# Kernel tuning notes

Measured on AMD Instinct MI355X. Metric: run time of the kernel, lower is better.

Reference implementation:

```python
import jax, jax.numpy as jnp
import numpy as np

NUM_HEADS = 16
NUM_KV_HEADS = 8
HEAD_DIM = 128
GATE_LOW_RANK = 16
GATE_NORMALIZER = 16.0
NORM_EPS = 1e-5
CHUNK = 64


def gla_chunk(q, k, v, g, chunk=CHUNK):
    """Chunkwise-parallel gated linear attention.
    q,k,v,g: [B,H,L,D]. Recurrence: S_t = diag(exp(g_t)) S_{t-1} + k_t^T v_t; o_t = q_t S_t.
    """
    B, H, L, D = q.shape
    n = L // chunk

    def rs(x):  # -> [n, B, H, C, D]
        return x.reshape(B, H, n, chunk, D).transpose(2, 0, 1, 3, 4)

    qc, kc, vc, gc = rs(q), rs(k), rs(v), rs(g)
    causal = jnp.tril(jnp.ones((chunk, chunk), dtype=bool))

    def step(S, inp):
        qt, kt, vt, gt = inp                      # [B,H,C,D]
        b = jnp.cumsum(gt, axis=-2)               # inclusive cumulative log-gates
        q_ = qt * jnp.exp(b)
        k_ = kt * jnp.exp(-b)
        # intra-chunk causal attention (diag included)
        A = jnp.einsum('bhid,bhjd->bhij', q_, k_)
        A = jnp.where(causal, A, 0.0)
        o = jnp.einsum('bhij,bhje->bhie', A, vt)
        # inter-chunk contribution from carried state
        o = o + jnp.einsum('bhid,bhde->bhie', q_, S)
        # state update to end of chunk
        k_end = kt * jnp.exp(b[..., -1:, :] - b)
        S_new = S * jnp.exp(b[..., -1, :])[..., None] + jnp.einsum('bhcd,bhce->bhde', k_end, vt)
        return S_new, o

    S0 = jnp.zeros((B, H, D, D), q.dtype)
    _, o = jax.lax.scan(step, S0, (qc, kc, vc, gc))
    return o.transpose(1, 2, 0, 3, 4).reshape(B, H, L, D)


def setup_inputs() -> dict:
    key = jax.random.key(0)
    ks = jax.random.split(key, 10)
    B, L, HID = 2, 2048, 2048
    KV = NUM_KV_HEADS * HEAD_DIM  # 1024
    w = 0.02
    return {
        'hidden_states': jax.random.normal(ks[0], (B, L, HID), jnp.float32),
        'Wq': jax.random.normal(ks[1], (HID, HID), jnp.float32) * w,
        'bq': jnp.zeros((HID,), jnp.float32),
        'Wk': jax.random.normal(ks[2], (HID, KV), jnp.float32) * w,
        'bk': jnp.zeros((KV,), jnp.float32),
        'Wv': jax.random.normal(ks[3], (HID, KV), jnp.float32) * w,
        'bv': jnp.zeros((KV,), jnp.float32),
        'Wg1': jax.random.normal(ks[4], (HID, GATE_LOW_RANK), jnp.float32) * w,
        'Wg2': jax.random.normal(ks[5], (GATE_LOW_RANK, KV), jnp.float32) * w,
        'bg2': jnp.zeros((KV,), jnp.float32),
        'g_norm_w': jnp.ones((HEAD_DIM,), jnp.float32),
        'Wo': jax.random.normal(ks[6], (HID, HID), jnp.float32) * w,
    }


def reference(hidden_states, Wq, bq, Wk, bk, Wv, bv, Wg1, Wg2, bg2, g_norm_w, Wo):
    B, L, HID = hidden_states.shape
    H, HKV, D = NUM_HEADS, NUM_KV_HEADS, HEAD_DIM
    n_rep = H // HKV

    q = jax.nn.relu(hidden_states @ Wq + bq)          # feature_map = relu
    k = jax.nn.relu(hidden_states @ Wk + bk)
    v = hidden_states @ Wv + bv
    gk = jax.nn.log_sigmoid((hidden_states @ Wg1) @ Wg2 + bg2) / GATE_NORMALIZER

    q = q.reshape(B, L, H, D).transpose(0, 2, 1, 3)    # [B,H,L,D]
    def to_heads(x):
        return x.reshape(B, L, HKV, D).transpose(0, 2, 1, 3)
    k, v, gk = to_heads(k), to_heads(v), to_heads(gk)  # [B,HKV,L,D]
    # GQA: repeat kv heads
    k = jnp.repeat(k, n_rep, axis=1)
    v = jnp.repeat(v, n_rep, axis=1)
    gk = jnp.repeat(gk, n_rep, axis=1)

    q = q * (D ** -0.5)                                # scale as in chunk_gla
    o = gla_chunk(q, k, v, gk)                         # [B,H,L,D]

    # per-head RMSNorm over head_dim
    o = o * jax.lax.rsqrt(jnp.mean(o * o, axis=-1, keepdims=True) + NORM_EPS) * g_norm_w
    o = o.transpose(0, 2, 1, 3).reshape(B, L, H * D)
    return o @ Wo
```

## Files before the change

kernel.cpp:

```cpp
#include <hip/hip_runtime.h>

typedef unsigned short u16;
typedef u16 u16x8 __attribute__((ext_vector_type(8)));
typedef u16 u16x4 __attribute__((ext_vector_type(4)));
typedef __bf16 bf16x8 __attribute__((ext_vector_type(8)));
typedef float f32x4 __attribute__((ext_vector_type(4)));

#define DEVI static __device__ __forceinline__

DEVI float b2f(u16 u){ union { unsigned u; float f; } c; c.u = ((unsigned)u) << 16; return c.f; }
DEVI u16 f2b(float f){ union { float f; unsigned u; } c; c.f = f;
  unsigned r = c.u + 0x7fffu + ((c.u >> 16) & 1u); return (u16)(r >> 16); }
DEVI void gload16(const void* g, void* l){
  __builtin_amdgcn_global_load_lds((const __attribute__((address_space(1))) void*)g,
                                   (__attribute__((address_space(3))) void*)l, 16, 0, 0);
}
DEVI f32x4 MFMA(bf16x8 a, bf16x8 b, f32x4 c){
  return __builtin_amdgcn_mfma_f32_16x16x32_bf16(a, b, c, 0, 0, 0);
}
#define WAITV(n) asm volatile("s_waitcnt vmcnt(" #n ")" ::: "memory")
#define WAITL0() asm volatile("s_waitcnt lgkmcnt(0)" ::: "memory")

constexpr size_t OFF_HB  = 0;
constexpr size_t OFF_WCT = OFF_HB  + (size_t)4096*2048*2;
constexpr size_t OFF_WOT = OFF_WCT + (size_t)4224*2048*2;
constexpr size_t OFF_QKV = OFF_WOT + (size_t)2048*2048*2;
constexpr size_t OFF_G1  = OFF_QKV + (size_t)4096*4096*2;
constexpr size_t OFF_G   = OFF_G1  + (size_t)4096*16*4;
constexpr size_t OFF_EB  = OFF_G   + (size_t)4096*1024*4;
constexpr size_t OFF_KD  = OFF_EB  + (size_t)4096*1024*2;
constexpr size_t OFF_T   = OFF_KD  + (size_t)4096*1024*2;
constexpr size_t OFF_DV  = OFF_T   + (size_t)2*8*32*128*128*2;
constexpr size_t OFF_SP  = OFF_DV  + (size_t)2*8*32*128*4;
constexpr size_t OFF_ON  = OFF_SP  + (size_t)2*8*32*128*128*2;

__global__ __launch_bounds__(256) void k_conv_h(const float* __restrict__ h, u16* __restrict__ hb){
  int idx = blockIdx.x*256 + threadIdx.x, stride = gridDim.x*256;
  for (int i = idx; i < 4096*2048/4; i += stride){
    float4 v = ((const float4*)h)[i];
    u16x4 o; o[0]=f2b(v.x); o[1]=f2b(v.y); o[2]=f2b(v.z); o[3]=f2b(v.w);
    ((u16x4*)hb)[i] = o;
  }
}

__global__ __launch_bounds__(256) void k_transpose(const float* __restrict__ src, u16* __restrict__ dst,
                                                   int K, int N, int rowOff, int pitch){
  __shared__ float tile[64][65];
  int kb = blockIdx.y*64, nb = blockIdx.x*64;
  int t = threadIdx.x, x = t & 63, y0 = t >> 6;
#pragma unroll
  for (int i = 0; i < 16; i++){
    int y = y0 + i*4, k = kb + y, n = nb + x;
    tile[y][x] = (n < N) ? src[(size_t)k*N + n] : 0.f;
  }
  __syncthreads();
#pragma unroll
  for (int i = 0; i < 16; i++){
    int y = y0 + i*4, n = nb + y, k = kb + x;
    if (n < N) dst[(size_t)(rowOff + n)*pitch + k] = f2b(tile[x][y]);
  }
}

__global__ __launch_bounds__(256) void k_wtilde(const float* __restrict__ Wg1, const float* __restrict__ Wg2,
                                                u16* __restrict__ wt){
  __shared__ float w2s[16*8];
  int c0 = blockIdx.x*8, t = threadIdx.x;
  if (t < 128){ int j = t>>3, cc = t&7; w2s[j*8+cc] = Wg2[j*1024 + c0 + cc]; }
  __syncthreads();
  int r0 = t*8;
#pragma unroll
  for (int half = 0; half < 2; half++){
    float rowv[4][16];
#pragma unroll
    for (int u = 0; u < 4; u++)
#pragma unroll
      for (int j4 = 0; j4 < 4; j4++)
        *(float4*)&rowv[u][j4*4] = *(const float4*)&Wg1[(size_t)(r0 + half*4 + u)*16 + j4*4];
#pragma unroll
    for (int cc = 0; cc < 8; cc++){
      u16x4 o;
#pragma unroll
      for (int u = 0; u < 4; u++){
        float s = 0.f;
#pragma unroll
        for (int j = 0; j < 16; j++) s += rowv[u][j]*w2s[j*8+cc];
        o[u] = f2b(s);
      }
      *(u16x4*)&wt[(size_t)(c0+cc)*2048 + r0 + half*4] = o;
    }
  }
}

template<int BM, int MODE>
__global__ __launch_bounds__(512, 2) void gemm256(const u16* __restrict__ A, const u16* __restrict__ Bt,
                                                  u16* __restrict__ Cq, float* __restrict__ Cf,
                                                  const float* __restrict__ bq, const float* __restrict__ bk,
                                                  const float* __restrict__ bv){
  constexpr int NT = 64;
  constexpr int MI = BM/32;
  constexpr int ALOADS = BM/128;
  constexpr int NTN = (MODE==0) ? 16 : 8;
  __shared__ u16 sA[4*BM*32];
  __shared__ u16 sB[4*256*32];
  int id = blockIdx.x;
  int swz = (id & 7)*32 + (id >> 3);
  int mt = swz / NTN, nt = swz % NTN;
  int t = threadIdx.x, w = t >> 6, l = t & 63;
  int wr = w >> 2, wc = w & 3;
  int mRow0 = mt*BM, nCol0 = nt*256;
  const u16* srcA[ALOADS]; const u16* srcB[2];
#pragma unroll
  for (int i = 0; i < ALOADS; i++){
    int S = t + i*512, r = S>>2, g = (S&3) ^ ((r>>1)&3);
    srcA[i] = A + (size_t)(mRow0 + r)*2048 + g*8;
  }
#pragma unroll
  for (int i = 0; i < 2; i++){
    int S = t + i*512, r = S>>2, g = (S&3) ^ ((r>>1)&3);
    srcB[i] = Bt + (size_t)(nCol0 + r)*2048 + g*8;
  }
  auto ISSUE = [&](int T){
    int buf = T & 3;
    u16* dA = sA + buf*(BM*32);
    u16* dB = sB + buf*(256*32);
#pragma unroll
    for (int i = 0; i < ALOADS; i++) gload16(srcA[i] + T*32, dA + (i*512 + w*64)*8);
#pragma unroll
    for (int i = 0; i < 2; i++)      gload16(srcB[i] + T*32, dB + (i*512 + w*64)*8);
  };
  f32x4 acc[MI][4] = {};
  ISSUE(0); ISSUE(1); ISSUE(2);
  for (int T = 0; T < NT; ++T){
    if (T + 3 < NT) ISSUE(T + 3);
    if constexpr (BM == 256){
      if (T < NT-3)       WAITV(12);
      else if (T == NT-3) WAITV(8);
      else if (T == NT-2) WAITV(4);
      else                WAITV(0);
    } else {
      if (T < NT-3)       WAITV(9);
      else if (T == NT-3) WAITV(6);
      else if (T == NT-2) WAITV(3);
      else                WAITV(0);
    }
    __builtin_amdgcn_s_barrier();
    const u16* bufA = sA + (T&3)*(BM*32);
    const u16* bufB = sB + (T&3)*(256*32);
    bf16x8 bfr[4], afr[MI];
#pragma unroll
    for (int ni = 0; ni < 4; ni++){
      int r = wc*64 + ni*16 + (l&15);
      int p = (l>>4) ^ ((r>>1)&3);
      bfr[ni] = *(const bf16x8*)&bufB[(r*4 + p)*8];
    }
#pragma unroll
    for (int mi = 0; mi < MI; mi++){
      int r = wr*(BM/2) + mi*16 + (l&15);
      int p = (l>>4) ^ ((r>>1)&3);
      afr[mi] = *(const bf16x8*)&bufA[(r*4 + p)*8];
    }
    __builtin_amdgcn_s_setprio(1);
#pragma unroll
    for (int mi = 0; mi < MI; mi++)
#pragma unroll
      for (int ni = 0; ni < 4; ni++)
        acc[mi][ni] = MFMA(afr[mi], bfr[ni], acc[mi][ni]);
    __builtin_amdgcn_s_setprio(0);
    WAITL0();
    __builtin_amdgcn_s_barrier();
  }
  int iLoc = (l>>4)*4, jc = l & 15;
  if (MODE == 0){
#pragma unroll
    for (int ni = 0; ni < 4; ni++){
      int n0 = nCol0 + wc*64 + ni*16;
      int n = n0 + jc;
      int kind; float bias;
      if (n0 < 2048){ kind = 0; bias = bq[n]; }
      else if (n0 < 3072){ kind = 1; bias = bk[n - 2048]; }
      else { kind = 2; bias = bv[n - 3072]; }
#pragma unroll
      for (int mi = 0; mi < MI; mi++){
        int m = mRow0 + wr*(BM/2) + mi*16 + iLoc;
#pragma unroll
        for (int rr = 0; rr < 4; rr++){
          float x = acc[mi][ni][rr] + bias;
          int row = m + rr;
          if (kind == 0)      Cq[(size_t)row*4096 + n] = f2b(fmaxf(x, 0.f) * 0.08838834764831845f);
          else if (kind == 1) Cq[(size_t)row*4096 + n] = f2b(fmaxf(x, 0.f));
          else                Cq[(size_t)row*4096 + n] = f2b(x);
        }
      }
    }
  } else {
#pragma unroll
    for (int ni = 0; ni < 4; ni++){
      int n = nCol0 + wc*64 + ni*16 + jc;
#pragma unroll
      for (int mi = 0; mi < MI; mi++){
        int m = mRow0 + wr*(BM/2) + mi*16 + iLoc;
#pragma unroll
        for (int rr = 0; rr < 4; rr++) Cf[(size_t)(m+rr)*2048 + n] = acc[mi][ni][rr];
      }
    }
  }
}

__global__ __launch_bounds__(256, 2) void gemmG(const u16* __restrict__ A, const u16* __restrict__ Bt,
                                                float* __restrict__ Cg, const float* __restrict__ bg2){
  constexpr int NT = 64;
  __shared__ u16 sA[4*128*32];
  __shared__ u16 sB[4*128*32];
  int id = blockIdx.x;
  int swz = (id & 7)*32 + (id >> 3);
  int mt = swz >> 3, nt = swz & 7;
  int t = threadIdx.x, w = t >> 6, l = t & 63;
  int wr = w >> 1, wc = w & 1;
  int mRow0 = mt*128, nCol0 = nt*128;
  const u16* srcA[2]; const u16* srcB[2];
#pragma unroll
  for (int i = 0; i < 2; i++){
    int S = t + i*256, r = S>>2, g = (S&3) ^ ((r>>1)&3);
    srcA[i] = A + (size_t)(mRow0 + r)*2048 + g*8;
    srcB[i] = Bt + (size_t)(nCol0 + r)*2048 + g*8;
  }
  auto ISSUE = [&](int T){
    int buf = T & 3;
    u16* dA = sA + buf*4096;
    u16* dB = sB + buf*4096;
#pragma unroll
    for (int i = 0; i < 2; i++) gload16(srcA[i] + T*32, dA + (i*256 + w*64)*8);
#pragma unroll
    for (int i = 0; i < 2; i++) gload16(srcB[i] + T*32, dB + (i*256 + w*64)*8);
  };
  f32x4 acc[4][4] = {};
  ISSUE(0); ISSUE(1); ISSUE(2);
  for (int T = 0; T < NT; ++T){
    if (T + 3 < NT) ISSUE(T + 3);
    if (T < NT-3)       WAITV(12);
    else if (T == NT-3) WAITV(8);
    else if (T == NT-2) WAITV(4);
    else                WAITV(0);
    __builtin_amdgcn_s_barrier();
    const u16* bufA = sA + (T&3)*4096;
    const u16* bufB = sB + (T&3)*4096;
    bf16x8 bfr[4], afr[4];
#pragma unroll
    for (int ni = 0; ni < 4; ni++){
      int r = wc*64 + ni*16 + (l&15);
      int p = (l>>4) ^ ((r>>1)&3);
      bfr[ni] = *(const bf16x8*)&bufB[(r*4 + p)*8];
    }
#pragma unroll
    for (int mi = 0; mi < 4; mi++){
      int r = wr*64 + mi*16 + (l&15);
      int p = (l>>4) ^ ((r>>1)&3);
      afr[mi] = *(const bf16x8*)&bufA[(r*4 + p)*8];
    }
    __builtin_amdgcn_s_setprio(1);
#pragma unroll
    for (int mi = 0; mi < 4; mi++)
#pragma unroll
      for (int ni = 0; ni < 4; ni++)
        acc[mi][ni] = MFMA(afr[mi], bfr[ni], acc[mi][ni]);
    __builtin_amdgcn_s_setprio(0);
    WAITL0();
    __builtin_amdgcn_s_barrier();
  }
  int iLoc = (l>>4)*4, jc = l & 15;
#pragma unroll
  for (int ni = 0; ni < 4; ni++){
    int n = nCol0 + wc*64 + ni*16 + jc;
    float bias = bg2[n];
#pragma unroll
    for (int mi = 0; mi < 4; mi++){
      int m = mRow0 + wr*64 + mi*16 + iLoc;
#pragma unroll
      for (int rr = 0; rr < 4; rr++) Cg[(size_t)(m+rr)*1024 + n] = acc[mi][ni][rr] + bias;
    }
  }
}

__global__ __launch_bounds__(256) void k_phaseA(const float* __restrict__ g, const u16* __restrict__ QKV,
                                                u16* __restrict__ eb, u16* __restrict__ kd,
                                                u16* __restrict__ T, float* __restrict__ Dv){
  __shared__ float gb[64*128];
  __shared__ u16 keT[128*72];
  __shared__ u16 vT [128*72];
  int c = blockIdx.x, kvh = blockIdx.y, b = blockIdx.z;
  int t = threadIdx.x;
  int tok0 = b*2048 + c*64;
#pragma unroll
  for (int r = 0; r < 8; r++){
    int idx4 = r*256 + t;
    int i = idx4 >> 5, c4 = idx4 & 31;
    float4 v = *(const float4*)&g[(size_t)(tok0+i)*1024 + kvh*128 + c4*4];
    float4 o;
    o.x = (fminf(v.x,0.f) - log1pf(expf(-fabsf(v.x)))) * 0.0625f;
    o.y = (fminf(v.y,0.f) - log1pf(expf(-fabsf(v.y)))) * 0.0625f;
    o.z = (fminf(v.z,0.f) - log1pf(expf(-fabsf(v.z)))) * 0.0625f;
    o.w = (fminf(v.w,0.f) - log1pf(expf(-fabsf(v.w)))) * 0.0625f;
    ((float4*)gb)[i*32 + c4] = o;
  }
  __syncthreads();
  if (t < 128){
    float run = 0.f;
    for (int i = 0; i < 64; i++){ run += gb[i*128 + t]; gb[i*128 + t] = run; }
    Dv[((size_t)(b*8+kvh)*32 + c)*128 + t] = expf(run);
  }
  __syncthreads();
  int d0 = (t&15)*8;
  float blast[8];
#pragma unroll
  for (int j = 0; j < 8; j++) blast[j] = gb[63*128 + d0 + j];
#pragma unroll
  for (int r = 0; r < 4; r++){
    int i = (t>>4) + r*16;
    u16x8 kv_ = *(const u16x8*)&QKV[(size_t)(tok0+i)*4096 + 2048 + kvh*128 + d0];
    u16x8 vv  = *(const u16x8*)&QKV[(size_t)(tok0+i)*4096 + 3072 + kvh*128 + d0];
    u16x8 ebv, kdv;
#pragma unroll
    for (int j = 0; j < 8; j++){
      float bcur = gb[i*128 + d0 + j];
      float kf = b2f(kv_[j]);
      ebv[j] = f2b(expf(bcur));
      kdv[j] = f2b(kf * expf(-bcur));
      keT[(d0+j)*72 + i] = f2b(kf * expf(blast[j] - bcur));
      vT [(d0+j)*72 + i] = vv[j];
    }
    *(u16x8*)&eb[(size_t)(tok0+i)*1024 + kvh*128 + d0] = ebv;
    *(u16x8*)&kd[(size_t)(tok0+i)*1024 + kvh*128 + d0] = kdv;
  }
  __syncthreads();
  int w = t>>6, l = t&63;
  f32x4 acc[2][8] = {};
#pragma unroll
  for (int ks = 0; ks < 2; ks++){
    bf16x8 af[2];
#pragma unroll
    for (int ti = 0; ti < 2; ti++)
      af[ti] = *(const bf16x8*)&keT[(w*32 + ti*16 + (l&15))*72 + ks*32 + (l>>4)*8];
#pragma unroll
    for (int tj = 0; tj < 8; tj++){
      bf16x8 bf_ = *(const bf16x8*)&vT[(tj*16 + (l&15))*72 + ks*32 + (l>>4)*8];
#pragma unroll
      for (int ti = 0; ti < 2; ti++) acc[ti][tj] = MFMA(af[ti], bf_, acc[ti][tj]);
    }
  }
  size_t tbase = ((size_t)(b*8+kvh)*32 + c)*16384;
#pragma unroll
  for (int ti = 0; ti < 2; ti++)
#pragma unroll
    for (int tj = 0; tj < 8; tj++)
#pragma unroll
      for (int rr = 0; rr < 4; rr++){
        int d = w*32 + ti*16 + (l>>4)*4 + rr, e = tj*16 + (l&15);
        T[tbase + d*128 + e] = f2b(acc[ti][tj][rr]);
      }
}

__global__ __launch_bounds__(256) void k_phaseB(const u16* __restrict__ T, const float* __restrict__ Dv,
                                                u16* __restrict__ SP){
  __shared__ u16 sl[16*128];
  int es = blockIdx.x, kvh = blockIdx.y, b = blockIdx.z;
  int t = threadIdx.x;
  size_t bh = (size_t)(b*8 + kvh);
  float S[8] = {0,0,0,0,0,0,0,0};
  for (int c = 0; c < 32; c++){
#pragma unroll
    for (int r = 0; r < 8; r++){
      int idx = r*256 + t, d = idx>>4, el = idx&15;
      sl[el*128 + d] = f2b(S[r]);
    }
    __syncthreads();
    size_t spb = (bh*32 + c)*16384 + (size_t)es*2048;
    *(u16x8*)&SP[spb + t*8] = *(const u16x8*)&sl[t*8];
    size_t tb  = (bh*32 + c)*16384;
    size_t dvb = (bh*32 + c)*128;
#pragma unroll
    for (int r = 0; r < 8; r++){
      int idx = r*256 + t, d = idx>>4, el = idx&15;
      float tv = b2f(T[tb + d*128 + es*16 + el]);
      S[r] = S[r]*Dv[dvb + d] + tv;
    }
    __syncthreads();
  }
}

__global__ __launch_bounds__(256) void k_phaseC(const u16* __restrict__ QKV, const u16* __restrict__ eb,
                                                const u16* __restrict__ kd, const u16* __restrict__ SP,
                                                const float* __restrict__ gnw, u16* __restrict__ onrm){
  __shared__ u16 kl[64*128];
  __shared__ u16 sl[64*72];
  __shared__ u16 vT[128*72];
  int c = blockIdx.x, h = blockIdx.y, b = blockIdx.z;
  int kvh = h >> 1;
  int t = threadIdx.x, w = t>>6, l = t&63;
  int tok0 = b*2048 + c*64;
#pragma unroll
  for (int is = 0; is < 4; is++){
    int row = (t>>4) + is*16;
    int d0s = 8*((t&15) ^ (row&7));
    gload16(&kd[(size_t)(tok0+row)*1024 + kvh*128 + d0s], &kl[is*2048 + w*512]);
  }
  int d0v = (t&15)*8;
#pragma unroll
  for (int r = 0; r < 4; r++){
    int i = (t>>4) + r*16;
    u16x8 vv = *(const u16x8*)&QKV[(size_t)(tok0+i)*4096 + 3072 + kvh*128 + d0v];
#pragma unroll
    for (int jj = 0; jj < 8; jj++) vT[(d0v+jj)*72 + i] = vv[jj];
  }
  bf16x8 aq[4];
  {
    int i = w*16 + (l&15);
#pragma unroll
    for (int kt = 0; kt < 4; kt++){
      int dq = kt*32 + (l>>4)*8;
      u16x8 qv = *(const u16x8*)&QKV[(size_t)(tok0+i)*4096 + h*128 + dq];
      u16x8 ev = *(const u16x8*)&eb[(size_t)(tok0+i)*1024 + kvh*128 + dq];
      u16x8 o;
#pragma unroll
      for (int jj = 0; jj < 8; jj++) o[jj] = f2b(b2f(qv[jj]) * b2f(ev[jj]));
      aq[kt] = __builtin_bit_cast(bf16x8, o);
    }
  }
  __syncthreads();
  f32x4 accs[4] = {};
#pragma unroll
  for (int kt = 0; kt < 4; kt++){
#pragma unroll
    for (int jt = 0; jt < 4; jt++){
      int j = jt*16 + (l&15);
      int byte_ = j*256 + ((2*(kt*32 + (l>>4)*8)) ^ ((j&7)<<4));
      bf16x8 bk_ = *(const bf16x8*)((const char*)kl + byte_);
      accs[jt] = MFMA(aq[kt], bk_, accs[jt]);
    }
  }
#pragma unroll
  for (int jt = 0; jt < 4; jt++)
#pragma unroll
    for (int rr = 0; rr < 4; rr++){
      int i = w*16 + (l>>4)*4 + rr;
      int j = jt*16 + (l&15);
      sl[i*72 + j] = f2b((i >= j) ? accs[jt][rr] : 0.f);
    }
  f32x4 acco[8] = {};
  size_t spb = ((size_t)(b*8+kvh)*32 + c)*16384;
#pragma unroll
  for (int kt = 0; kt < 4; kt++){
#pragma unroll
    for (int et = 0; et < 8; et++){
      int e = et*16 + (l&15);
      int dd = kt*32 + (l>>4)*8;
      bf16x8 bs = *(const bf16x8*)&SP[spb + (size_t)e*128 + dd];
      acco[et] = MFMA(aq[kt], bs, acco[et]);
    }
  }
#pragma unroll
  for (int kt2 = 0; kt2 < 2; kt2++){
    int i = w*16 + (l&15);
    bf16x8 as = *(const bf16x8*)&sl[i*72 + kt2*32 + (l>>4)*8];
#pragma unroll
    for (int et = 0; et < 8; et++){
      bf16x8 bv_ = *(const bf16x8*)&vT[(et*16 + (l&15))*72 + kt2*32 + (l>>4)*8];
      acco[et] = MFMA(as, bv_, acco[et]);
    }
  }
  float gw[8];
#pragma unroll
  for (int et = 0; et < 8; et++) gw[et] = gnw[et*16 + (l&15)];
#pragma unroll
  for (int rr = 0; rr < 4; rr++){
    int i = w*16 + (l>>4)*4 + rr;
    float ss = 0.f;
#pragma unroll
    for (int et = 0; et < 8; et++){ float x = acco[et][rr]; ss += x*x; }
    ss += __shfl_xor(ss, 1); ss += __shfl_xor(ss, 2);
    ss += __shfl_xor(ss, 4); ss += __shfl_xor(ss, 8);
    float sc = rsqrtf(ss*(1.f/128.f) + 1e-5f);
#pragma unroll
    for (int et = 0; et < 8; et++){
      int e = et*16 + (l&15);
      onrm[(size_t)(tok0+i)*2048 + h*128 + e] = f2b(acco[et][rr]*sc*gw[et]);
    }
  }
}

extern "C" void kernel_launch(void* const* d_in, const int* in_sizes, int n_in,
                              void* d_out, int out_size, void* d_ws, size_t ws_size,
                              hipStream_t stream){
  (void)in_sizes; (void)n_in; (void)out_size; (void)ws_size;
  const float* h   = (const float*)d_in[0];
  const float* Wq  = (const float*)d_in[1];
  const float* bq  = (const float*)d_in[2];
  const float* Wk  = (const float*)d_in[3];
  const float* bk  = (const float*)d_in[4];
  const float* Wv  = (const float*)d_in[5];
  const float* bv  = (const float*)d_in[6];
  const float* Wg1 = (const float*)d_in[7];
  const float* Wg2 = (const float*)d_in[8];
  const float* bg2 = (const float*)d_in[9];
  const float* gnw = (const float*)d_in[10];
  const float* Wo  = (const float*)d_in[11];
  float* out = (float*)d_out;
  char* ws = (char*)d_ws;
  u16*   hb   = (u16*)  (ws + OFF_HB);
  u16*   wct  = (u16*)  (ws + OFF_WCT);
  u16*   wot  = (u16*)  (ws + OFF_WOT);
  u16*   qkv  = (u16*)  (ws + OFF_QKV);
  float* gbuf = (float*)(ws + OFF_G);
  u16*   ebuf = (u16*)  (ws + OFF_EB);
  u16*   kdb  = (u16*)  (ws + OFF_KD);
  u16*   Tb   = (u16*)  (ws + OFF_T);
  u16*   wtilT= (u16*)  (ws + OFF_T);
  float* Dvb  = (float*)(ws + OFF_DV);
  u16*   SPb  = (u16*)  (ws + OFF_SP);
  u16*   onb  = (u16*)  (ws + OFF_ON);

  k_conv_h<<<2048, 256, 0, stream>>>(h, hb);
  k_transpose<<<dim3(32,32), 256, 0, stream>>>(Wq,  wct, 2048, 2048,    0, 2048);
  k_transpose<<<dim3(16,32), 256, 0, stream>>>(Wk,  wct, 2048, 1024, 2048, 2048);
  k_transpose<<<dim3(16,32), 256, 0, stream>>>(Wv,  wct, 2048, 1024, 3072, 2048);
  k_transpose<<<dim3(32,32), 256, 0, stream>>>(Wo,  wot, 2048, 2048,    0, 2048);
  k_wtilde<<<128, 256, 0, stream>>>(Wg1, Wg2, wtilT);
  gemm256<256,0><<<256, 512, 0, stream>>>(hb, wct, qkv, nullptr, bq, bk, bv);
  gemmG<<<256, 256, 0, stream>>>(hb, wtilT, gbuf, bg2);
  k_phaseA<<<dim3(32,8,2), 256, 0, stream>>>(gbuf, qkv, ebuf, kdb, Tb, Dvb);
  k_phaseB<<<dim3(8,8,2), 256, 0, stream>>>(Tb, Dvb, SPb);
  k_phaseC<<<dim3(32,16,2), 256, 0, stream>>>(qkv, ebuf, kdb, SPb, gnw, onb);
  gemm256<128,1><<<256, 512, 0, stream>>>(onb, wot, nullptr, out, nullptr, nullptr, nullptr);
}
```

Measured before the change: 475.8 us.

## Unify GEMMs into 128x128 double-buffered kernel and transpose state layout for phaseB

Replaces the 256-wide 4-stage GEMM kernels and the separate gate GEMM with one 128x128-tile kernel that uses 256 threads, 2-stage double buffering and __syncthreads, and launches more blocks. Phase A now writes the chunk state transposed (e-major), so phase B can drop its shared-memory transpose and barriers and use vectorized 8-wide loads and stores per thread. The GEMM change trades reuse per block and prefetch depth for occupancy, and may expose more memory latency than the 4-stage pipeline did. Phase C must read the state in the new transposed layout.

```diff
diff --git a/kernel.cpp b/kernel.cpp
--- a/kernel.cpp
+++ b/kernel.cpp
@@ -18,8 +18,6 @@
 DEVI f32x4 MFMA(bf16x8 a, bf16x8 b, f32x4 c){
   return __builtin_amdgcn_mfma_f32_16x16x32_bf16(a, b, c, 0, 0, 0);
 }
-#define WAITV(n) asm volatile("s_waitcnt vmcnt(" #n ")" ::: "memory")
-#define WAITL0() asm volatile("s_waitcnt lgkmcnt(0)" ::: "memory")
 
 constexpr size_t OFF_HB  = 0;
 constexpr size_t OFF_WCT = OFF_HB  + (size_t)4096*2048*2;
@@ -91,62 +89,46 @@
   }
 }
 
-template<int BM, int MODE>
-__global__ __launch_bounds__(512, 2) void gemm256(const u16* __restrict__ A, const u16* __restrict__ Bt,
+template<int MODE>
+__global__ __launch_bounds__(256, 4) void gemm128(const u16* __restrict__ A, const u16* __restrict__ Bt,
                                                   u16* __restrict__ Cq, float* __restrict__ Cf,
                                                   const float* __restrict__ bq, const float* __restrict__ bk,
-                                                  const float* __restrict__ bv){
+                                                  const float* __restrict__ bv, const float* __restrict__ bg2){
   constexpr int NT = 64;
-  constexpr int MI = BM/32;
-  constexpr int ALOADS = BM/128;
-  constexpr int NTN = (MODE==0) ? 16 : 8;
-  __shared__ u16 sA[4*BM*32];
-  __shared__ u16 sB[4*256*32];
+  constexpr int NTN = (MODE==0) ? 32 : (MODE==1) ? 16 : 8;
+  constexpr int CPX = (MODE==0) ? 128 : (MODE==1) ? 64 : 32;
+  __shared__ u16 sA[2*128*32];
+  __shared__ u16 sB[2*128*32];
   int id = blockIdx.x;
-  int swz = (id & 7)*32 + (id >> 3);
+  int swz = (id & 7)*CPX + (id >> 3);
   int mt = swz / NTN, nt = swz % NTN;
   int t = threadIdx.x, w = t >> 6, l = t & 63;
-  int wr = w >> 2, wc = w & 3;
-  int mRow0 = mt*BM, nCol0 = nt*256;
-  const u16* srcA[ALOADS]; const u16* srcB[2];
-#pragma unroll
-  for (int i = 0; i < ALOADS; i++){
-    int S = t + i*512, r = S>>2, g = (S&3) ^ ((r>>1)&3);
+  int wr = w >> 1, wc = w & 1;
+  int mRow0 = mt*128, nCol0 = nt*128;
+  const u16* srcA[2]; const u16* srcB[2];
+#pragma unroll
+  for (int i = 0; i < 2; i++){
+    int S = t + i*256, r = S>>2, g = (S&3) ^ ((r>>1)&3);
     srcA[i] = A + (size_t)(mRow0 + r)*2048 + g*8;
-  }
-#pragma unroll
-  for (int i = 0; i < 2; i++){
-    int S = t + i*512, r = S>>2, g = (S&3) ^ ((r>>1)&3);
     srcB[i] = Bt + (size_t)(nCol0 + r)*2048 + g*8;
   }
   auto ISSUE = [&](int T){
-    int buf = T & 3;
-    u16* dA = sA + buf*(BM*32);
-    u16* dB = sB + buf*(256*32);
-#pragma unroll
-    for (int i = 0; i < ALOADS; i++) gload16(srcA[i] + T*32, dA + (i*512 + w*64)*8);
-#pragma unroll
-    for (int i = 0; i < 2; i++)      gload16(srcB[i] + T*32, dB + (i*512 + w*64)*8);
+    int buf = T & 1;
+    u16* dA = sA + buf*4096;
+    u16* dB = sB + buf*4096;
+#pragma unroll
+    for (int i = 0; i < 2; i++) gload16(srcA[i] + T*32, dA + (i*256 + w*64)*8);
+#pragma unroll
+    for (int i = 0; i < 2; i++) gload16(srcB[i] + T*32, dB + (i*256 + w*64)*8);
   };
-  f32x4 acc[MI][4] = {};
-  ISSUE(0); ISSUE(1); ISSUE(2);
+  f32x4 acc[4][4] = {};
+  ISSUE(0);
   for (int T = 0; T < NT; ++T){
-    if (T + 3 < NT) ISSUE(T + 3);
-    if constexpr (BM == 256){
-      if (T < NT-3)       WAITV(12);
-      else if (T == NT-3) WAITV(8);
-      else if (T == NT-2) WAITV(4);
-      else                WAITV(0);
-    } else {
-      if (T < NT-3)       WAITV(9);
-      else if (T == NT-3) WAITV(6);
-      else if (T == NT-2) WAITV(3);
-      else                WAITV(0);
-    }
-    __builtin_amdgcn_s_barrier();
-    const u16* bufA = sA + (T&3)*(BM*32);
-    const u16* bufB = sB + (T&3)*(256*32);
-    bf16x8 bfr[4], afr[MI];
+    __syncthreads();
+    if (T + 1 < NT) ISSUE(T + 1);
+    const u16* bufA = sA + (T&1)*4096;
+    const u16* bufB = sB + (T&1)*4096;
+    bf16x8 bfr[4], afr[4];
 #pragma unroll
     for (int ni = 0; ni < 4; ni++){
       int r = wc*64 + ni*16 + (l&15);
@@ -154,34 +136,29 @@
       bfr[ni] = *(const bf16x8*)&bufB[(r*4 + p)*8];
     }
 #pragma unroll
-    for (int mi = 0; mi < MI; mi++){
-      int r = wr*(BM/2) + mi*16 + (l&15);
+    for (int mi = 0; mi < 4; mi++){
+      int r = wr*64 + mi*16 + (l&15);
       int p = (l>>4) ^ ((r>>1)&3);
       afr[mi] = *(const bf16x8*)&bufA[(r*4 + p)*8];
     }
     __builtin_amdgcn_s_setprio(1);
 #pragma unroll
-    for (int mi = 0; mi < MI; mi++)
+    for (int mi = 0; mi < 4; mi++)
 #pragma unroll
       for (int ni = 0; ni < 4; ni++)
         acc[mi][ni] = MFMA(afr[mi], bfr[ni], acc[mi][ni]);
     __builtin_amdgcn_s_setprio(0);
-    WAITL0();
-    __builtin_amdgcn_s_barrier();
   }
   int iLoc = (l>>4)*4, jc = l & 15;
   if (MODE == 0){
+    int kind = (nt < 16) ? 0 : (nt < 24) ? 1 : 2;
 #pragma unroll
     for (int ni = 0; ni < 4; ni++){
-      int n0 = nCol0 + wc*64 + ni*16;
-      int n = n0 + jc;
-      int kind; float bias;
-      if (n0 < 2048){ kind = 0; bias = bq[n]; }
-      else if (n0 < 3072){ kind = 1; bias = bk[n - 2048]; }
-      else { kind = 2; bias = bv[n - 3072]; }
-#pragma unroll
-      for (int mi = 0; mi < MI; mi++){
-        int m = mRow0 + wr*(BM/2) + mi*16 + iLoc;
+      int n = nCol0 + wc*64 + ni*16 + jc;
+      float bias = (kind == 0) ? bq[n] : (kind == 1) ? bk[n - 2048] : bv[n - 3072];
+#pragma unroll
+      for (int mi = 0; mi < 4; mi++){
+        int m = mRow0 + wr*64 + mi*16 + iLoc;
 #pragma unroll
         for (int rr = 0; rr < 4; rr++){
           float x = acc[mi][ni][rr] + bias;
@@ -192,91 +169,28 @@
         }
       }
     }
-  } else {
+  } else if (MODE == 1){
 #pragma unroll
     for (int ni = 0; ni < 4; ni++){
       int n = nCol0 + wc*64 + ni*16 + jc;
 #pragma unroll
-      for (int mi = 0; mi < MI; mi++){
-        int m = mRow0 + wr*(BM/2) + mi*16 + iLoc;
+      for (int mi = 0; mi < 4; mi++){
+        int m = mRow0 + wr*64 + mi*16 + iLoc;
 #pragma unroll
         for (int rr = 0; rr < 4; rr++) Cf[(size_t)(m+rr)*2048 + n] = acc[mi][ni][rr];
       }
     }
-  }
-}
-
-__global__ __launch_bounds__(256, 2) void gemmG(const u16* __restrict__ A, const u16* __restrict__ Bt,
-                                                float* __restrict__ Cg, const float* __restrict__ bg2){
-  constexpr int NT = 64;
-  __shared__ u16 sA[4*128*32];
-  __shared__ u16 sB[4*128*32];
-  int id = blockIdx.x;
-  int swz = (id & 7)*32 + (id >> 3);
-  int mt = swz >> 3, nt = swz & 7;
-  int t = threadIdx.x, w = t >> 6, l = t & 63;
-  int wr = w >> 1, wc = w & 1;
-  int mRow0 = mt*128, nCol0 = nt*128;
-  const u16* srcA[2]; const u16* srcB[2];
-#pragma unroll
-  for (int i = 0; i < 2; i++){
-    int S = t + i*256, r = S>>2, g = (S&3) ^ ((r>>1)&3);
-    srcA[i] = A + (size_t)(mRow0 + r)*2048 + g*8;
-    srcB[i] = Bt + (size_t)(nCol0 + r)*2048 + g*8;
-  }
-  auto ISSUE = [&](int T){
-    int buf = T & 3;
-    u16* dA = sA + buf*4096;
-    u16* dB = sB + buf*4096;
-#pragma unroll
-    for (int i = 0; i < 2; i++) gload16(srcA[i] + T*32, dA + (i*256 + w*64)*8);
-#pragma unroll
-    for (int i = 0; i < 2; i++) gload16(srcB[i] + T*32, dB + (i*256 + w*64)*8);
-  };
-  f32x4 acc[4][4] = {};
-  ISSUE(0); ISSUE(1); ISSUE(2);
-  for (int T = 0; T < NT; ++T){
-    if (T + 3 < NT) ISSUE(T + 3);
-    if (T < NT-3)       WAITV(12);
-    else if (T == NT-3) WAITV(8);
-    else if (T == NT-2) WAITV(4);
-    else                WAITV(0);
-    __builtin_amdgcn_s_barrier();
-    const u16* bufA = sA + (T&3)*4096;
-    const u16* bufB = sB + (T&3)*4096;
-    bf16x8 bfr[4], afr[4];
+  } else {
 #pragma unroll
     for (int ni = 0; ni < 4; ni++){
-      int r = wc*64 + ni*16 + (l&15);
-      int p = (l>>4) ^ ((r>>1)&3);
-      bfr[ni] = *(const bf16x8*)&bufB[(r*4 + p)*8];
-    }
-#pragma unroll
-    for (int mi = 0; mi < 4; mi++){
-      int r = wr*64 + mi*16 + (l&15);
-      int p = (l>>4) ^ ((r>>1)&3);
-      afr[mi] = *(const bf16x8*)&bufA[(r*4 + p)*8];
-    }
-    __builtin_amdgcn_s_setprio(1);
-#pragma unroll
-    for (int mi = 0; mi < 4; mi++)
-#pragma unroll
-      for (int ni = 0; ni < 4; ni++)
-        acc[mi][ni] = MFMA(afr[mi], bfr[ni], acc[mi][ni]);
-    __builtin_amdgcn_s_setprio(0);
-    WAITL0();
-    __builtin_amdgcn_s_barrier();
-  }
-  int iLoc = (l>>4)*4, jc = l & 15;
-#pragma unroll
-  for (int ni = 0; ni < 4; ni++){
-    int n = nCol0 + wc*64 + ni*16 + jc;
-    float bias = bg2[n];
-#pragma unroll
-    for (int mi = 0; mi < 4; mi++){
-      int m = mRow0 + wr*64 + mi*16 + iLoc;
-#pragma unroll
-      for (int rr = 0; rr < 4; rr++) Cg[(size_t)(m+rr)*1024 + n] = acc[mi][ni][rr] + bias;
+      int n = nCol0 + wc*64 + ni*16 + jc;
+      float bias = bg2[n];
+#pragma unroll
+      for (int mi = 0; mi < 4; mi++){
+        int m = mRow0 + wr*64 + mi*16 + iLoc;
+#pragma unroll
+        for (int rr = 0; rr < 4; rr++) Cf[(size_t)(m+rr)*1024 + n] = acc[mi][ni][rr] + bias;
+      }
     }
   }
 }
@@ -338,52 +252,47 @@
   for (int ks = 0; ks < 2; ks++){
     bf16x8 af[2];
 #pragma unroll
-    for (int ti = 0; ti < 2; ti++)
-      af[ti] = *(const bf16x8*)&keT[(w*32 + ti*16 + (l&15))*72 + ks*32 + (l>>4)*8];
-#pragma unroll
-    for (int tj = 0; tj < 8; tj++){
-      bf16x8 bf_ = *(const bf16x8*)&vT[(tj*16 + (l&15))*72 + ks*32 + (l>>4)*8];
-#pragma unroll
-      for (int ti = 0; ti < 2; ti++) acc[ti][tj] = MFMA(af[ti], bf_, acc[ti][tj]);
+    for (int te = 0; te < 2; te++)
+      af[te] = *(const bf16x8*)&vT[(w*32 + te*16 + (l&15))*72 + ks*32 + (l>>4)*8];
+#pragma unroll
+    for (int td = 0; td < 8; td++){
+      bf16x8 bf_ = *(const bf16x8*)&keT[(td*16 + (l&15))*72 + ks*32 + (l>>4)*8];
+#pragma unroll
+      for (int te = 0; te < 2; te++) acc[te][td] = MFMA(af[te], bf_, acc[te][td]);
     }
   }
   size_t tbase = ((size_t)(b*8+kvh)*32 + c)*16384;
 #pragma unroll
-  for (int ti = 0; ti < 2; ti++)
-#pragma unroll
-    for (int tj = 0; tj < 8; tj++)
+  for (int te = 0; te < 2; te++)
+#pragma unroll
+    for (int td = 0; td < 8; td++)
 #pragma unroll
       for (int rr = 0; rr < 4; rr++){
-        int d = w*32 + ti*16 + (l>>4)*4 + rr, e = tj*16 + (l&15);
-        T[tbase + d*128 + e] = f2b(acc[ti][tj][rr]);
+        int e = w*32 + te*16 + (l>>4)*4 + rr, d = td*16 + (l&15);
+        T[tbase + e*128 + d] = f2b(acc[te][td][rr]);
       }
 }
 
 __global__ __launch_bounds__(256) void k_phaseB(const u16* __restrict__ T, const float* __restrict__ Dv,
                                                 u16* __restrict__ SP){
-  __shared__ u16 sl[16*128];
-  int es = blockIdx.x, kvh = blockIdx.y, b = blockIdx.z;
+  int kvh = blockIdx.y, b = blockIdx.z;
   int t = threadIdx.x;
-  size_t bh = (size_t)(b*8 + kvh);
+  int e = blockIdx.x*16 + (t >> 4);
+  int d0 = (t & 15)*8;
+  size_t base = ((size_t)(b*8 + kvh)*32)*16384 + (size_t)e*128 + d0;
+  size_t dvb  = ((size_t)(b*8 + kvh)*32)*128 + d0;
   float S[8] = {0,0,0,0,0,0,0,0};
   for (int c = 0; c < 32; c++){
-#pragma unroll
-    for (int r = 0; r < 8; r++){
-      int idx = r*256 + t, d = idx>>4, el = idx&15;
-      sl[el*128 + d] = f2b(S[r]);
-    }
-    __syncthreads();
-    size_t spb = (bh*32 + c)*16384 + (size_t)es*2048;
-    *(u16x8*)&SP[spb + t*8] = *(const u16x8*)&sl[t*8];
-    size_t tb  = (bh*32 + c)*16384;
-    size_t dvb = (bh*32 + c)*128;
-#pragma unroll
-    for (int r = 0; r < 8; r++){
-      int idx = r*256 + t, d = idx>>4, el = idx&15;
-      float tv = b2f(T[tb + d*128 + es*16 + el]);
-      S[r] = S[r]*Dv[dvb + d] + tv;
-    }
-    __syncthreads();
+    u16x8 tv = *(const u16x8*)&T[base + (size_t)c*16384];
+    float4 dva = *(const float4*)&Dv[dvb + (size_t)c*128];
+    float4 dvbv = *(const float4*)&Dv[dvb + (size_t)c*128 + 4];
+    u16x8 o;
+#pragma unroll
+    for (int j = 0; j < 8; j++) o[j] = f2b(S[j]);
+    *(u16x8*)&SP[base + (size_t)c*16384] = o;
+    float dv[8] = {dva.x, dva.y, dva.z, dva.w, dvbv.x, dvbv.y, dvbv.z, dvbv.w};
+#pragma unroll
+    for (int j = 0; j < 8; j++) S[j] = S[j]*dv[j] + b2f(tv[j]);
   }
 }
 
@@ -524,10 +433,10 @@
   k_transpose<<<dim3(16,32), 256, 0, stream>>>(Wv,  wct, 2048, 1024, 3072, 2048);
   k_transpose<<<dim3(32,32), 256, 0, stream>>>(Wo,  wot, 2048, 2048,    0, 2048);
   k_wtilde<<<128, 256, 0, stream>>>(Wg1, Wg2, wtilT);
-  gemm256<256,0><<<256, 512, 0, stream>>>(hb, wct, qkv, nullptr, bq, bk, bv);
-  gemmG<<<256, 256, 0, stream>>>(hb, wtilT, gbuf, bg2);
+  gemm128<0><<<1024, 256, 0, stream>>>(hb, wct, qkv, nullptr, bq, bk, bv, nullptr);
+  gemm128<2><<<256, 256, 0, stream>>>(hb, wtilT, nullptr, gbuf, nullptr, nullptr, nullptr, bg2);
   k_phaseA<<<dim3(32,8,2), 256, 0, stream>>>(gbuf, qkv, ebuf, kdb, Tb, Dvb);
   k_phaseB<<<dim3(8,8,2), 256, 0, stream>>>(Tb, Dvb, SPb);
   k_phaseC<<<dim3(32,16,2), 256, 0, stream>>>(qkv, ebuf, kdb, SPb, gnw, onb);
-  gemm256<128,1><<<256, 512, 0, stream>>>(onb, wot, nullptr, out, nullptr, nullptr, nullptr);
-}
+  gemm128<1><<<512, 256, 0, stream>>>(onb, wot, nullptr, out, nullptr, nullptr, nullptr, nullptr);
+}
```

Measured after the change: 423.0 us. -11.1%, faster.
